# Kernel tuning notes

Hardware: AMD Instinct MI355X
Metric: run time of the kernel (lower is better)

Reference implementation:

```python
import jax, jax.numpy as jnp
import numpy as np

N = 50000
E = 800000
TEXT_VOCAB = 7000
ACTION_DIM = 64
MAX_POS = 5120
POS_DIM = 128   # edge encoder out_dim
NODE_DIM = 128  # text_out 64 + type_out 64
EDGE_DIM = 128
H1 = 256
OUT = 32
NEG_SLOPE = 0.2


def _pos_table():
    # sinusoidal table, [MAX_POS+1, POS_DIM]; even cols = cos, odd cols = sin
    positions = np.arange(0, MAX_POS + 1, dtype=np.float32)
    inv_freq = 1.0 / (10000.0 ** (np.arange(0.0, POS_DIM, 2.0, dtype=np.float32) / POS_DIM))
    si = np.outer(positions, inv_freq)
    tab = np.zeros((MAX_POS + 1, POS_DIM), dtype=np.float32)
    tab[:, 1::2] = np.sin(si)
    tab[:, 0::2] = np.cos(si)
    return jnp.asarray(tab)


def setup_inputs() -> dict:
    key = jax.random.key(0)
    ks = jax.random.split(key, 32)
    ri = jax.random.randint
    nrm = lambda k, s, scale=0.05: (jax.random.normal(k, s, dtype=jnp.float32) * scale)
    x = jnp.stack([ri(ks[0], (N,), 0, TEXT_VOCAB + 1, dtype=jnp.int32),
                   ri(ks[1], (N,), 0, 3, dtype=jnp.int32)], axis=-1)
    edge_index = ri(ks[2], (2, E), 0, N, dtype=jnp.int32)
    edge_attr = jnp.stack([ri(ks[3], (E,), 0, 3, dtype=jnp.int32),
                           ri(ks[4], (E,), 0, MAX_POS + 1, dtype=jnp.int32)], axis=-1)
    d = {
        "x": x, "edge_index": edge_index, "edge_attr": edge_attr,
        "text_emb": nrm(ks[5], (TEXT_VOCAB + 1, 64), 1.0),
        "type_emb": nrm(ks[6], (3, 64), 1.0),
        "flow_emb": nrm(ks[7], (3, EDGE_DIM), 1.0),
        "pos_table": _pos_table(),
        "pos_W": nrm(ks[8], (POS_DIM, POS_DIM)), "pos_b": nrm(ks[9], (POS_DIM,)),
        "c1_Wl": nrm(ks[10], (NODE_DIM, H1)), "c1_bl": nrm(ks[11], (H1,)),
        "c1_Wr": nrm(ks[12], (NODE_DIM, H1)), "c1_br": nrm(ks[13], (H1,)),
        "c1_We": nrm(ks[14], (EDGE_DIM, H1)), "c1_att": nrm(ks[15], (H1,)),
        "c1_bias": nrm(ks[16], (H1,)),
        "c2_Wl": nrm(ks[17], (H1, OUT)), "c2_bl": nrm(ks[18], (OUT,)),
        "c2_Wr": nrm(ks[19], (H1, OUT)), "c2_br": nrm(ks[20], (OUT,)),
        "c2_We": nrm(ks[21], (EDGE_DIM, OUT)), "c2_att": nrm(ks[22], (OUT,)),
        "c2_bias": nrm(ks[23], (OUT,)),
        "policy_W": nrm(ks[24], (OUT, ACTION_DIM), 0.2), "policy_b": nrm(ks[25], (ACTION_DIM,)),
    }
    return d


def gatv2(h, src, dst, ea, Wl, bl, Wr, br, We, att, bias, n):
    # PyG GATv2Conv, heads=1, add_self_loops=True, fill_value='mean'
    loop_attr = jnp.broadcast_to(ea.mean(0), (n, ea.shape[1]))
    s = jnp.concatenate([src, jnp.arange(n, dtype=src.dtype)])
    d = jnp.concatenate([dst, jnp.arange(n, dtype=dst.dtype)])
    ea_full = jnp.concatenate([ea, loop_attr], axis=0)
    xl = h @ Wl + bl  # messages (source side)
    xr = h @ Wr + br  # destination side
    m = xl[s] + xr[d] + ea_full @ We          # [E+n, F]
    e = jnp.where(m > 0, m, NEG_SLOPE * m) @ att  # per-edge logit [E+n]
    emax = jax.ops.segment_max(e, d, num_segments=n)
    a = jnp.exp(e - emax[d])
    denom = jax.ops.segment_sum(a, d, num_segments=n)
    alpha = a / denom[d]
    return jax.ops.segment_sum(alpha[:, None] * xl[s], d, num_segments=n) + bias


def reference(x, edge_index, edge_attr, text_emb, type_emb, flow_emb, pos_table,
              pos_W, pos_b,
              c1_Wl, c1_bl, c1_Wr, c1_br, c1_We, c1_att, c1_bias,
              c2_Wl, c2_bl, c2_Wr, c2_br, c2_We, c2_att, c2_bias,
              policy_W, policy_b):
    # NodeEncoder: concat of text and type embeddings -> [N, 128]
    h = jnp.concatenate([text_emb[x[:, 0]], type_emb[x[:, 1]]], axis=-1)
    # EdgeEncoder: flow embedding + linear(position sinusoid embedding)
    pos = edge_attr[:, 1]
    pos = jnp.where(pos > MAX_POS, pos, MAX_POS)  # faithful to original .where usage
    pos = jnp.clip(pos, 0, MAX_POS)
    ea = flow_emb[edge_attr[:, 0]] + (pos_table[pos] @ pos_W + pos_b)  # [E, 128]
    src, dst = edge_index[0], edge_index[1]
    h = gatv2(h, src, dst, ea, c1_Wl, c1_bl, c1_Wr, c1_br, c1_We, c1_att, c1_bias, h.shape[0])
    h = gatv2(h, src, dst, ea, c2_Wl, c2_bl, c2_Wr, c2_br, c2_We, c2_att, c2_bias, h.shape[0])
    g = h.mean(0)  # [32] graph readout
    logits = g @ policy_W + policy_b
    return jax.nn.softmax(logits, axis=-1)
```

## Files before the change

### kernel.cpp

```cpp
#include <hip/hip_runtime.h>

#define NEG_SLOPE 0.2f

typedef __attribute__((ext_vector_type(8))) short bf16x8;
typedef __attribute__((ext_vector_type(4))) float f32x4;

static __device__ __forceinline__ float wsum64(float v) {
#pragma unroll
    for (int off = 32; off >= 1; off >>= 1) v += __shfl_xor(v, off, 64);
    return v;
}
static __device__ __forceinline__ float wmax64(float v) {
#pragma unroll
    for (int off = 32; off >= 1; off >>= 1) v = fmaxf(v, __shfl_xor(v, off, 64));
    return v;
}

static __device__ __forceinline__ unsigned short bf16r(float a) {
    unsigned int u = __float_as_uint(a);
    return (unsigned short)((u + 0x7FFFu + ((u >> 16) & 1u)) >> 16);
}
static __device__ __forceinline__ unsigned int bf16pack(float a, float b) {
    unsigned int ua = __float_as_uint(a);
    ua = (ua + 0x7FFFu + ((ua >> 16) & 1u)) >> 16;
    unsigned int ub = __float_as_uint(b);
    ub = (ub + 0x7FFFu + ((ub >> 16) & 1u)) & 0xFFFF0000u;
    return ua | ub;
}
static __device__ __forceinline__ float4 bf16x4_to_f4(uint2 u) {
    float4 v;
    v.x = __uint_as_float(u.x << 16);
    v.y = __uint_as_float(u.x & 0xFFFF0000u);
    v.z = __uint_as_float(u.y << 16);
    v.w = __uint_as_float(u.y & 0xFFFF0000u);
    return v;
}

static __device__ __forceinline__ float sdot4(const float4 xs, const float4 pre,
                                              const float4 av6, const float4 av4) {
    float m0 = xs.x + pre.x, m1 = xs.y + pre.y;
    float m2 = xs.z + pre.z, m3 = xs.w + pre.w;
    float q = av6.x * m0 + av4.x * fabsf(m0);
    q = fmaf(av6.y, m1, q); q = fmaf(av4.y, fabsf(m1), q);
    q = fmaf(av6.z, m2, q); q = fmaf(av4.z, fabsf(m2), q);
    q = fmaf(av6.w, m3, q); q = fmaf(av4.w, fabsf(m3), q);
    return q;
}

__global__ void k_edges(const int* __restrict__ ei, const int* __restrict__ ea,
                        int* __restrict__ cntF, int* __restrict__ cnt3, int E) {
    __shared__ int sh3[3];
    if (threadIdx.x < 3) sh3[threadIdx.x] = 0;
    __syncthreads();
    int e = blockIdx.x * blockDim.x + threadIdx.x;
    if (e < E) {
        int dd = ei[E + e];
        int f = ea[2 * e];
        f = f < 0 ? 0 : (f > 2 ? 2 : f);
        atomicAdd(&cntF[dd * 3 + f], 1);
        atomicAdd(&sh3[f], 1);
    }
    __syncthreads();
    if (threadIdx.x < 3) atomicAdd(&cnt3[threadIdx.x], sh3[threadIdx.x]);
}

__global__ void k_prep_all(const float* __restrict__ pos_table, const float* __restrict__ pos_W,
                           const float* __restrict__ pos_b, const float* __restrict__ flow_emb,
                           const float* __restrict__ We1, const float* __restrict__ We2,
                           const int* __restrict__ cnt3,
                           float* __restrict__ eaW1, float* __restrict__ loopW1,
                           float* __restrict__ eaW2, float* __restrict__ loopW2,
                           const float* __restrict__ Wl1, const float* __restrict__ Wr1,
                           const float* __restrict__ Wl2, const float* __restrict__ Wr2,
                           unsigned short* __restrict__ Bt1, unsigned short* __restrict__ Bt2,
                           int E) {
    if (blockIdx.x != 0) {
        int i = (blockIdx.x - 1) * 256 + threadIdx.x;
        if (i < 512 * 128) {
            int nn = i >> 7, k = i & 127;
            float v = (nn < 256) ? Wl1[(size_t)k * 256 + nn] : Wr1[(size_t)k * 256 + nn - 256];
            Bt1[i] = bf16r(v);
        } else {
            int j = i - 512 * 128;
            if (j < 64 * 256) {
                int nn = j >> 8, k = j & 255;
                float v = (nn < 32) ? Wl2[(size_t)k * 32 + nn] : Wr2[(size_t)k * 32 + nn - 32];
                Bt2[j] = bf16r(v);
            }
        }
        return;
    }
    __shared__ float posc[128];
    __shared__ float lv[128];
    int t = threadIdx.x;
    if (t < 128) {
        const float* row = pos_table + 5120 * 128;
        float a = pos_b[t];
        for (int k = 0; k < 128; ++k) a += row[k] * pos_W[k * 128 + t];
        posc[t] = a;
        float invE = 1.0f / (float)E;
        lv[t] = ((float)cnt3[0] * flow_emb[t] + (float)cnt3[1] * flow_emb[128 + t] +
                 (float)cnt3[2] * flow_emb[256 + t]) * invE + a;
    }
    __syncthreads();
    {
        int j = t;
        float a0 = 0.f, a1 = 0.f, a2 = 0.f, al = 0.f;
        for (int k = 0; k < 128; ++k) {
            float w = We1[k * 256 + j];
            float pc = posc[k];
            a0 += (flow_emb[k] + pc) * w;
            a1 += (flow_emb[128 + k] + pc) * w;
            a2 += (flow_emb[256 + k] + pc) * w;
            al += lv[k] * w;
        }
        eaW1[j] = a0; eaW1[256 + j] = a1; eaW1[512 + j] = a2; loopW1[j] = al;
    }
    if (t < 32) {
        int j = t;
        float a0 = 0.f, a1 = 0.f, a2 = 0.f, al = 0.f;
        for (int k = 0; k < 128; ++k) {
            float w = We2[k * 32 + j];
            float pc = posc[k];
            a0 += (flow_emb[k] + pc) * w;
            a1 += (flow_emb[128 + k] + pc) * w;
            a2 += (flow_emb[256 + k] + pc) * w;
            al += lv[k] * w;
        }
        eaW2[j] = a0; eaW2[32 + j] = a1; eaW2[64 + j] = a2; loopW2[j] = al;
    }
}

__global__ __launch_bounds__(256) void k_scan_block(const int* __restrict__ cnt,
                                                    int* __restrict__ rowptr,
                                                    int* __restrict__ bsum, int n) {
    __shared__ int sh[256];
    int b = blockIdx.x, t = threadIdx.x;
    int base = b * 1024 + t * 4;
    int v0 = base + 0 < n ? cnt[base + 0] : 0;
    int v1 = base + 1 < n ? cnt[base + 1] : 0;
    int v2 = base + 2 < n ? cnt[base + 2] : 0;
    int v3 = base + 3 < n ? cnt[base + 3] : 0;
    int tot = v0 + v1 + v2 + v3;
    sh[t] = tot;
    __syncthreads();
    for (int off = 1; off < 256; off <<= 1) {
        int x = (t >= off) ? sh[t - off] : 0;
        __syncthreads();
        sh[t] += x;
        __syncthreads();
    }
    int excl = (t > 0) ? sh[t - 1] : 0;
    if (base + 0 < n) rowptr[base + 0] = excl;
    if (base + 1 < n) rowptr[base + 1] = excl + v0;
    if (base + 2 < n) rowptr[base + 2] = excl + v0 + v1;
    if (base + 3 < n) rowptr[base + 3] = excl + v0 + v1 + v2;
    if (t == 255) bsum[b] = sh[255];
}

__global__ void k_scan_top(int* __restrict__ bsum, int* __restrict__ rowptr, int nb, int n) {
    if (threadIdx.x == 0 && blockIdx.x == 0) {
        int run = 0;
        for (int b = 0; b < nb; ++b) { int x = bsum[b]; bsum[b] = run; run += x; }
        rowptr[n] = run;
    }
}

__global__ void k_scan_add(int* __restrict__ rowptr, const int* __restrict__ bsum,
                           int* __restrict__ wptr, int n) {
    int i = blockIdx.x * blockDim.x + threadIdx.x;
    if (i < n) {
        int v = rowptr[i] + bsum[i >> 10];
        rowptr[i] = v;
        wptr[i] = v;
    }
}

__global__ void k_scatter(const int* __restrict__ ei, const int* __restrict__ ea,
                          int* __restrict__ wptr, int* __restrict__ packed, int E) {
    int e = blockIdx.x * blockDim.x + threadIdx.x;
    if (e >= E) return;
    int s = ei[e], dd = ei[E + e];
    int f = ea[2 * e];
    f = f < 0 ? 0 : (f > 2 ? 2 : f);
    int p = atomicAdd(&wptr[dd * 3 + f], 1);
    packed[p] = s | (f << 16);
}

__global__ __launch_bounds__(256) void k_gemm1(const int* __restrict__ x,
        const float* __restrict__ text_emb, const float* __restrict__ type_emb,
        const unsigned short* __restrict__ Bt,
        const float* __restrict__ bl, const float* __restrict__ br,
        unsigned short* __restrict__ xc, int n) {
    __shared__ unsigned short Ash[64][136];
    __shared__ unsigned short Bsh[128][136];
    int t = threadIdx.x;
    int node0 = blockIdx.x * 64;
    for (int i = t; i < 64 * 128; i += 256) {
        int r = i >> 7, cc = i & 127;
        int nd = node0 + r;
        float v = 0.f;
        if (nd < n)
            v = (cc < 64) ? text_emb[(size_t)x[nd * 2] * 64 + cc]
                          : type_emb[(size_t)x[nd * 2 + 1] * 64 + (cc - 64)];
        Ash[r][cc] = bf16r(v);
    }
    int wave = t >> 6, lane = t & 63;
    int m = lane & 15, q = lane >> 4;
    for (int nb = 0; nb < 4; ++nb) {
        __syncthreads();
        for (int i = t; i < 128 * 16; i += 256) {
            int r = i >> 4, cs = i & 15;
            uint4 v = ((const uint4*)(Bt + (size_t)(nb * 128 + r) * 128))[cs];
            *(uint4*)&Bsh[r][cs * 8] = v;
        }
        __syncthreads();
        f32x4 acc[8];
#pragma unroll
        for (int nt = 0; nt < 8; ++nt) acc[nt] = (f32x4){0.f, 0.f, 0.f, 0.f};
#pragma unroll
        for (int k = 0; k < 128; k += 32) {
            bf16x8 a = *(const bf16x8*)&Ash[wave * 16 + m][k + q * 8];
#pragma unroll
            for (int nt = 0; nt < 8; ++nt) {
                bf16x8 b = *(const bf16x8*)&Bsh[nt * 16 + m][k + q * 8];
                acc[nt] = __builtin_amdgcn_mfma_f32_16x16x32_bf16(a, b, acc[nt], 0, 0, 0);
            }
        }
#pragma unroll
        for (int r = 0; r < 4; ++r) {
            int node = node0 + wave * 16 + q * 4 + r;
            if (node < n) {
                unsigned short* rowp = xc + (size_t)node * 512 + nb * 128 + m;
#pragma unroll
                for (int nt = 0; nt < 8; ++nt) {
                    int ng = nb * 128 + nt * 16 + m;
                    float bv = (ng < 256) ? bl[ng] : br[ng - 256];
                    rowp[nt * 16] = bf16r(acc[nt][r] + bv);
                }
            }
        }
    }
}

__global__ __launch_bounds__(256) void k_gemm2(const unsigned short* __restrict__ h2b,
        const unsigned short* __restrict__ Bt,
        const float* __restrict__ bl, const float* __restrict__ br,
        unsigned short* __restrict__ xc, int n) {
    __shared__ unsigned short Ash[32][264];
    __shared__ unsigned short Bsh[64][264];
    int t = threadIdx.x;
    int node0 = blockIdx.x * 32;
    for (int i = t; i < 32 * 32; i += 256) {
        int r = i >> 5, cs = i & 31;
        int nd = node0 + r;
        uint4 v = make_uint4(0u, 0u, 0u, 0u);
        if (nd < n) v = ((const uint4*)(h2b + (size_t)nd * 256))[cs];
        *(uint4*)&Ash[r][cs * 8] = v;
    }
    for (int i = t; i < 64 * 32; i += 256) {
        int r = i >> 5, cs = i & 31;
        uint4 v = ((const uint4*)(Bt + (size_t)r * 256))[cs];
        *(uint4*)&Bsh[r][cs * 8] = v;
    }
    __syncthreads();
    int wave = t >> 6, lane = t & 63;
    int m = lane & 15, q = lane >> 4;
    int mrow = (wave >> 1) * 16;
    int nh   = (wave & 1) * 32;
    f32x4 acc[2];
    acc[0] = (f32x4){0.f, 0.f, 0.f, 0.f};
    acc[1] = (f32x4){0.f, 0.f, 0.f, 0.f};
#pragma unroll
    for (int k = 0; k < 256; k += 32) {
        bf16x8 a = *(const bf16x8*)&Ash[mrow + m][k + q * 8];
#pragma unroll
        for (int nt = 0; nt < 2; ++nt) {
            bf16x8 b = *(const bf16x8*)&Bsh[nh + nt * 16 + m][k + q * 8];
            acc[nt] = __builtin_amdgcn_mfma_f32_16x16x32_bf16(a, b, acc[nt], 0, 0, 0);
        }
    }
#pragma unroll
    for (int r = 0; r < 4; ++r) {
        int node = node0 + mrow + q * 4 + r;
        if (node < n) {
#pragma unroll
            for (int nt = 0; nt < 2; ++nt) {
                int ng = nh + nt * 16 + m;
                float bv = (ng < 32) ? bl[ng] : br[ng - 32];
                xc[(size_t)node * 64 + ng] = bf16r(acc[nt][r] + bv);
            }
        }
    }
}

__global__ __launch_bounds__(256) void k_gat256(const unsigned short* __restrict__ xc1,
        const int* __restrict__ rowptrF, const int* __restrict__ packed,
        const float* __restrict__ eaW, const float* __restrict__ loopW,
        const float* __restrict__ att, const float* __restrict__ bias,
        unsigned short* __restrict__ h2b, int n) {
    int wid = (blockIdx.x * blockDim.x + threadIdx.x) >> 6;
    int lane = threadIdx.x & 63;
    if (wid >= n) return;
    int d = wid;
    int c = lane * 4;
    float4 xld = bf16x4_to_f4(((const uint2*)(xc1 + (size_t)d * 512))[lane]);
    float4 xrd = bf16x4_to_f4(((const uint2*)(xc1 + (size_t)d * 512 + 256))[lane]);
    float4 av = *(const float4*)(att + c);
    float4 av6, av4;
    av6.x = 0.6f * av.x; av6.y = 0.6f * av.y; av6.z = 0.6f * av.z; av6.w = 0.6f * av.w;
    av4.x = 0.4f * av.x; av4.y = 0.4f * av.y; av4.z = 0.4f * av.z; av4.w = 0.4f * av.w;
    float4 r0 = *(const float4*)(eaW + c);
    float4 r1 = *(const float4*)(eaW + 256 + c);
    float4 r2 = *(const float4*)(eaW + 512 + c);
    r0.x += xrd.x; r0.y += xrd.y; r0.z += xrd.z; r0.w += xrd.w;
    r1.x += xrd.x; r1.y += xrd.y; r1.z += xrd.z; r1.w += xrd.w;
    r2.x += xrd.x; r2.y += xrd.y; r2.z += xrd.z; r2.w += xrd.w;
    float den;
    float4 acc;
    {
        float4 lw = *(const float4*)(loopW + c);
        lw.x += xrd.x; lw.y += xrd.y; lw.z += xrd.z; lw.w += xrd.w;
        float q = wsum64(sdot4(xld, lw, av6, av4));
        float wself = __expf(q);
        den = wself;
        acc.x = wself * xld.x; acc.y = wself * xld.y;
        acc.z = wself * xld.z; acc.w = wself * xld.w;
    }
    int p = rowptrF[d * 3], p1 = rowptrF[d * 3 + 3];
    for (; p + 4 <= p1; p += 4) {
        int pk0 = packed[p],     pk1 = packed[p + 1];
        int pk2 = packed[p + 2], pk3 = packed[p + 3];
        uint2 u0 = ((const uint2*)(xc1 + (size_t)(pk0 & 0xFFFF) * 512))[lane];
        uint2 u1 = ((const uint2*)(xc1 + (size_t)(pk1 & 0xFFFF) * 512))[lane];
        uint2 u2 = ((const uint2*)(xc1 + (size_t)(pk2 & 0xFFFF) * 512))[lane];
        uint2 u3 = ((const uint2*)(xc1 + (size_t)(pk3 & 0xFFFF) * 512))[lane];
        float4 xs0 = bf16x4_to_f4(u0);
        float4 xs1 = bf16x4_to_f4(u1);
        float4 xs2 = bf16x4_to_f4(u2);
        float4 xs3 = bf16x4_to_f4(u3);
        int f0 = pk0 >> 16, f1 = pk1 >> 16, f2 = pk2 >> 16, f3 = pk3 >> 16;
        float4 pr0 = (f0 == 0) ? r0 : ((f0 == 1) ? r1 : r2);
        float4 pr1 = (f1 == 0) ? r0 : ((f1 == 1) ? r1 : r2);
        float4 pr2 = (f2 == 0) ? r0 : ((f2 == 1) ? r1 : r2);
        float4 pr3 = (f3 == 0) ? r0 : ((f3 == 1) ? r1 : r2);
        float q0 = sdot4(xs0, pr0, av6, av4);
        float q1 = sdot4(xs1, pr1, av6, av4);
        float q2 = sdot4(xs2, pr2, av6, av4);
        float q3 = sdot4(xs3, pr3, av6, av4);
#pragma unroll
        for (int off = 32; off >= 1; off >>= 1) {
            q0 += __shfl_xor(q0, off, 64);
            q1 += __shfl_xor(q1, off, 64);
            q2 += __shfl_xor(q2, off, 64);
            q3 += __shfl_xor(q3, off, 64);
        }
        float w0 = __expf(q0), w1 = __expf(q1);
        float w2 = __expf(q2), w3 = __expf(q3);
        den += (w0 + w1) + (w2 + w3);
        acc.x += w0 * xs0.x + w1 * xs1.x + w2 * xs2.x + w3 * xs3.x;
        acc.y += w0 * xs0.y + w1 * xs1.y + w2 * xs2.y + w3 * xs3.y;
        acc.z += w0 * xs0.z + w1 * xs1.z + w2 * xs2.z + w3 * xs3.z;
        acc.w += w0 * xs0.w + w1 * xs1.w + w2 * xs2.w + w3 * xs3.w;
    }
    for (; p < p1; ++p) {
        int pk = packed[p];
        float4 xs = bf16x4_to_f4(((const uint2*)(xc1 + (size_t)(pk & 0xFFFF) * 512))[lane]);
        int f = pk >> 16;
        float4 pr = (f == 0) ? r0 : ((f == 1) ? r1 : r2);
        float qq = wsum64(sdot4(xs, pr, av6, av4));
        float w = __expf(qq);
        den += w;
        acc.x += w * xs.x; acc.y += w * xs.y; acc.z += w * xs.z; acc.w += w * xs.w;
    }
    float inv = 1.f / den;
    float4 bv = *(const float4*)(bias + c);
    float ox = fmaf(acc.x, inv, bv.x), oy = fmaf(acc.y, inv, bv.y);
    float oz = fmaf(acc.z, inv, bv.z), ow = fmaf(acc.w, inv, bv.w);
    ((uint2*)(h2b + (size_t)d * 256))[lane] = make_uint2(bf16pack(ox, oy), bf16pack(oz, ow));
}

__global__ __launch_bounds__(256) void k_gat32(const unsigned short* __restrict__ xc2,
        const int* __restrict__ rowptrF, const int* __restrict__ packed,
        const float* __restrict__ eaW, const float* __restrict__ loopW,
        const float* __restrict__ att, const float* __restrict__ bias,
        float* __restrict__ out, int n) {
    int wid = (blockIdx.x * blockDim.x + threadIdx.x) >> 6;
    if (wid >= n) return;
    int lane = threadIdx.x & 63;
    int g = lane >> 4, li = lane & 15;
    int d = wid;
    unsigned int uxl = ((const unsigned int*)(xc2 + (size_t)d * 64))[li];
    unsigned int uxr = ((const unsigned int*)(xc2 + (size_t)d * 64 + 32))[li];
    float xl0 = __uint_as_float(uxl << 16), xl1 = __uint_as_float(uxl & 0xFFFF0000u);
    float xr0 = __uint_as_float(uxr << 16), xr1 = __uint_as_float(uxr & 0xFFFF0000u);
    float2 avv = ((const float2*)att)[li];
    float a60 = 0.6f * avv.x, a61 = 0.6f * avv.y;
    float a40 = 0.4f * avv.x, a41 = 0.4f * avv.y;
    float2 e0 = ((const float2*)eaW)[li];
    float2 e1 = ((const float2*)(eaW + 32))[li];
    float2 e2 = ((const float2*)(eaW + 64))[li];
    float p00 = e0.x + xr0, p01 = e0.y + xr1;
    float p10 = e1.x + xr0, p11 = e1.y + xr1;
    float p20 = e2.x + xr0, p21 = e2.y + xr1;
    float den, acc0, acc1;
    {
        float2 lwv = ((const float2*)loopW)[li];
        float m0 = xl0 + xr0 + lwv.x, m1 = xl1 + xr1 + lwv.y;
        float q = a60 * m0 + a40 * fabsf(m0);
        q = fmaf(a61, m1, q); q = fmaf(a41, fabsf(m1), q);
        q += __shfl_xor(q, 1, 64); q += __shfl_xor(q, 2, 64);
        q += __shfl_xor(q, 4, 64); q += __shfl_xor(q, 8, 64);
        float wself = __expf(q);
        den  = (g == 0) ? wself : 0.f;
        acc0 = (g == 0) ? wself * xl0 : 0.f;
        acc1 = (g == 0) ? wself * xl1 : 0.f;
    }
    int pA = rowptrF[d * 3], pB = rowptrF[d * 3 + 3];
    int p = pA + g;
    for (; p + 4 < pB; p += 8) {
        int pk0 = packed[p], pk1 = packed[p + 4];
        unsigned int ua = ((const unsigned int*)(xc2 + (size_t)(pk0 & 0xFFFF) * 64))[li];
        unsigned int ub = ((const unsigned int*)(xc2 + (size_t)(pk1 & 0xFFFF) * 64))[li];
        int fA = pk0 >> 16, fB = pk1 >> 16;
        float preA0 = (fA == 0) ? p00 : ((fA == 1) ? p10 : p20);
        float preA1 = (fA == 0) ? p01 : ((fA == 1) ? p11 : p21);
        float preB0 = (fB == 0) ? p00 : ((fB == 1) ? p10 : p20);
        float preB1 = (fB == 0) ? p01 : ((fB == 1) ? p11 : p21);
        float xa0 = __uint_as_float(ua << 16), xa1 = __uint_as_float(ua & 0xFFFF0000u);
        float xb0 = __uint_as_float(ub << 16), xb1 = __uint_as_float(ub & 0xFFFF0000u);
        float ma0 = xa0 + preA0, ma1 = xa1 + preA1;
        float mb0 = xb0 + preB0, mb1 = xb1 + preB1;
        float qa = a60 * ma0 + a40 * fabsf(ma0);
        qa = fmaf(a61, ma1, qa); qa = fmaf(a41, fabsf(ma1), qa);
        float qb = a60 * mb0 + a40 * fabsf(mb0);
        qb = fmaf(a61, mb1, qb); qb = fmaf(a41, fabsf(mb1), qb);
#pragma unroll
        for (int off = 1; off <= 8; off <<= 1) {
            qa += __shfl_xor(qa, off, 64);
            qb += __shfl_xor(qb, off, 64);
        }
        float wa = __expf(qa), wb = __expf(qb);
        den += wa + wb;
        acc0 = fmaf(wb, xb0, fmaf(wa, xa0, acc0));
        acc1 = fmaf(wb, xb1, fmaf(wa, xa1, acc1));
    }
    for (; p < pB; p += 4) {
        int pk = packed[p];
        unsigned int u = ((const unsigned int*)(xc2 + (size_t)(pk & 0xFFFF) * 64))[li];
        int f = pk >> 16;
        float pre0 = (f == 0) ? p00 : ((f == 1) ? p10 : p20);
        float pre1 = (f == 0) ? p01 : ((f == 1) ? p11 : p21);
        float x0 = __uint_as_float(u << 16), x1 = __uint_as_float(u & 0xFFFF0000u);
        float m0 = x0 + pre0, m1 = x1 + pre1;
        float q = a60 * m0 + a40 * fabsf(m0);
        q = fmaf(a61, m1, q); q = fmaf(a41, fabsf(m1), q);
        q += __shfl_xor(q, 1, 64); q += __shfl_xor(q, 2, 64);
        q += __shfl_xor(q, 4, 64); q += __shfl_xor(q, 8, 64);
        float w = __expf(q);
        den += w;
        acc0 = fmaf(w, x0, acc0);
        acc1 = fmaf(w, x1, acc1);
    }
    acc0 += __shfl_xor(acc0, 16, 64); acc0 += __shfl_xor(acc0, 32, 64);
    acc1 += __shfl_xor(acc1, 16, 64); acc1 += __shfl_xor(acc1, 32, 64);
    den  += __shfl_xor(den, 16, 64);  den  += __shfl_xor(den, 32, 64);
    if (g == 0) {
        float2 bvv = ((const float2*)bias)[li];
        float inv = 1.f / den;
        float2 o;
        o.x = fmaf(acc0, inv, bvv.x);
        o.y = fmaf(acc1, inv, bvv.y);
        ((float2*)(out + (size_t)d * 32))[li] = o;
    }
}

__global__ __launch_bounds__(256) void k_mean(const float* __restrict__ out2,
                                              float* __restrict__ gsum, int n) {
    __shared__ float sh[256];
    int t = threadIdx.x;
    int c = t & 31, g = t >> 5;
    float acc = 0.f;
    for (int nd = blockIdx.x * 8 + g; nd < n; nd += gridDim.x * 8)
        acc += out2[(size_t)nd * 32 + c];
    sh[t] = acc;
    __syncthreads();
    if (t < 32) {
        float s2 = 0.f;
#pragma unroll
        for (int gg = 0; gg < 8; ++gg) s2 += sh[gg * 32 + c];
        atomicAdd(&gsum[c], s2);
    }
}

__global__ void k_final(const float* __restrict__ gsum, const float* __restrict__ policy_W,
                        const float* __restrict__ policy_b, float* __restrict__ out, int n) {
    int t = threadIdx.x;
    float invN = 1.0f / (float)n;
    float acc = policy_b[t];
    for (int cc = 0; cc < 32; ++cc) acc += gsum[cc] * invN * policy_W[cc * 64 + t];
    float mx = wmax64(acc);
    float ex = __expf(acc - mx);
    float s = wsum64(ex);
    out[t] = ex / s;
}

extern "C" void kernel_launch(void* const* d_in, const int* in_sizes, int n_in,
                              void* d_out, int out_size, void* d_ws, size_t ws_size,
                              hipStream_t stream) {
    const int* x          = (const int*)d_in[0];
    const int* edge_index = (const int*)d_in[1];
    const int* edge_attr  = (const int*)d_in[2];
    const float* text_emb = (const float*)d_in[3];
    const float* type_emb = (const float*)d_in[4];
    const float* flow_emb = (const float*)d_in[5];
    const float* pos_table= (const float*)d_in[6];
    const float* pos_W    = (const float*)d_in[7];
    const float* pos_b    = (const float*)d_in[8];
    const float* c1_Wl    = (const float*)d_in[9];
    const float* c1_bl    = (const float*)d_in[10];
    const float* c1_Wr    = (const float*)d_in[11];
    const float* c1_br    = (const float*)d_in[12];
    const float* c1_We    = (const float*)d_in[13];
    const float* c1_att   = (const float*)d_in[14];
    const float* c1_bias  = (const float*)d_in[15];
    const float* c2_Wl    = (const float*)d_in[16];
    const float* c2_bl    = (const float*)d_in[17];
    const float* c2_Wr    = (const float*)d_in[18];
    const float* c2_br    = (const float*)d_in[19];
    const float* c2_We    = (const float*)d_in[20];
    const float* c2_att   = (const float*)d_in[21];
    const float* c2_bias  = (const float*)d_in[22];
    const float* policy_W = (const float*)d_in[23];
    const float* policy_b = (const float*)d_in[24];
    float* out = (float*)d_out;

    const int N = in_sizes[0] / 2;
    const int E = in_sizes[1] / 2;
    const int n3 = 3 * N;

    char* base = (char*)d_ws;
    size_t off = 0;
    auto alloc = [&](size_t bytes) -> void* {
        void* p = base + off;
        off = (off + bytes + 255) & ~(size_t)255;
        return p;
    };
    unsigned short* xc1  = (unsigned short*)alloc((size_t)N * 512 * 2);
    unsigned short* h2b  = (unsigned short*)alloc((size_t)N * 256 * 2);
    unsigned short* xc2  = (unsigned short*)alloc((size_t)N * 64 * 2);
    float*          out2 = (float*)alloc((size_t)N * 32 * 4);
    unsigned short* Bt1  = (unsigned short*)alloc((size_t)512 * 128 * 2);
    unsigned short* Bt2  = (unsigned short*)alloc((size_t)64 * 256 * 2);
    int*            zreg   = (int*)alloc((size_t)(n3 + 36) * 4);
    int*            cntF   = zreg;
    int*            cnt3   = zreg + n3;
    float*          gsum   = (float*)(zreg + n3 + 4);
    int*            rowptrF= (int*)alloc((size_t)(n3 + 1) * 4);
    int*            packed = (int*)alloc((size_t)E * 4);
    int*            bsum   = (int*)alloc(256 * 4);
    float*          eaW1   = (float*)alloc(768 * 4);
    float*          loopW1 = (float*)alloc(256 * 4);
    float*          eaW2   = (float*)alloc(96 * 4);
    float*          loopW2 = (float*)alloc(32 * 4);

    hipMemsetAsync(zreg, 0, (size_t)(n3 + 36) * 4, stream);

    k_edges<<<(E + 255) / 256, 256, 0, stream>>>(edge_index, edge_attr, cntF, cnt3, E);
    k_prep_all<<<1 + (512 * 128 + 64 * 256) / 256, 256, 0, stream>>>(
        pos_table, pos_W, pos_b, flow_emb, c1_We, c2_We, cnt3,
        eaW1, loopW1, eaW2, loopW2, c1_Wl, c1_Wr, c2_Wl, c2_Wr, Bt1, Bt2, E);

    int nb = (n3 + 1023) / 1024;
    k_scan_block<<<nb, 256, 0, stream>>>(cntF, rowptrF, bsum, n3);
    k_scan_top<<<1, 64, 0, stream>>>(bsum, rowptrF, nb, n3);
    k_scan_add<<<(n3 + 255) / 256, 256, 0, stream>>>(rowptrF, bsum, cntF, n3);
    k_scatter<<<(E + 255) / 256, 256, 0, stream>>>(edge_index, edge_attr, cntF, packed, E);

    k_gemm1<<<(N + 63) / 64, 256, 0, stream>>>(x, text_emb, type_emb, Bt1,
                                               c1_bl, c1_br, xc1, N);
    k_gat256<<<(N + 3) / 4, 256, 0, stream>>>(xc1, rowptrF, packed, eaW1, loopW1,
                                              c1_att, c1_bias, h2b, N);

    k_gemm2<<<(N + 31) / 32, 256, 0, stream>>>(h2b, Bt2, c2_bl, c2_br, xc2, N);
    k_gat32<<<(N + 3) / 4, 256, 0, stream>>>(xc2, rowptrF, packed, eaW2, loopW2,
                                             c2_att, c2_bias, out2, N);

    k_mean<<<256, 256, 0, stream>>>(out2, gsum, N);
    k_final<<<1, 64, 0, stream>>>(gsum, policy_W, policy_b, out, N);
}
```

Before: 431.6 us.

## Split leaky-relu attention score into precomputed linear part and abs part

Uses leaky_relu(m)=0.6m+0.4|m| to move the linear term of the layer-1 attention score into per-node (alpha) and per-flow-type (delta) scalars, computed by a new k_alpha256 kernel. The per-edge inner loop then only evaluates the abs term plus a scalar gather, and the log2e scaling is folded in so exp2f can replace __expf. It also adds readfirstlane on the node index and a uniform-flow fast path. The cost is an extra kernel launch, an N-float buffer, and one extra scalar gather per edge.

```diff
diff --git a/kernel.cpp b/kernel.cpp
--- a/kernel.cpp
+++ b/kernel.cpp
@@ -1,9 +1,9 @@
 #include <hip/hip_runtime.h>
-
-#define NEG_SLOPE 0.2f
 
 typedef __attribute__((ext_vector_type(8))) short bf16x8;
 typedef __attribute__((ext_vector_type(4))) float f32x4;
+
+#define L2E 1.4426950408889634f
 
 static __device__ __forceinline__ float wsum64(float v) {
 #pragma unroll
@@ -35,15 +35,18 @@
     v.w = __uint_as_float(u.y & 0xFFFF0000u);
     return v;
 }
-
-static __device__ __forceinline__ float sdot4(const float4 xs, const float4 pre,
-                                              const float4 av6, const float4 av4) {
+static __device__ __forceinline__ float rflf(float v) {
+    return __int_as_float(__builtin_amdgcn_readfirstlane(__float_as_int(v)));
+}
+
+static __device__ __forceinline__ float adot4(const float4 xs, const float4 pre,
+                                              const float4 av4) {
     float m0 = xs.x + pre.x, m1 = xs.y + pre.y;
     float m2 = xs.z + pre.z, m3 = xs.w + pre.w;
-    float q = av6.x * m0 + av4.x * fabsf(m0);
-    q = fmaf(av6.y, m1, q); q = fmaf(av4.y, fabsf(m1), q);
-    q = fmaf(av6.z, m2, q); q = fmaf(av4.z, fabsf(m2), q);
-    q = fmaf(av6.w, m3, q); q = fmaf(av4.w, fabsf(m3), q);
+    float q = av4.x * fabsf(m0);
+    q = fmaf(av4.y, fabsf(m1), q);
+    q = fmaf(av4.z, fabsf(m2), q);
+    q = fmaf(av4.w, fabsf(m3), q);
     return q;
 }
 
@@ -294,35 +297,69 @@
     }
 }
 
+__global__ __launch_bounds__(256) void k_alpha256(const unsigned short* __restrict__ xc1,
+        const float* __restrict__ att, const float* __restrict__ eaW,
+        const float* __restrict__ loopW, float* __restrict__ alpha,
+        float* __restrict__ delta, int n) {
+    const float S6 = 0.6f * L2E;
+    int lane = threadIdx.x & 63;
+    int c = lane * 4;
+    float4 av = *(const float4*)(att + c);
+    int wid = (blockIdx.x * blockDim.x + threadIdx.x) >> 6;
+    if (wid < n) {
+        float4 xl = bf16x4_to_f4(((const uint2*)(xc1 + (size_t)wid * 512))[lane]);
+        float q = av.x * xl.x;
+        q = fmaf(av.y, xl.y, q); q = fmaf(av.z, xl.z, q); q = fmaf(av.w, xl.w, q);
+        q = wsum64(q);
+        if (lane == 0) alpha[wid] = q * S6;
+    } else if (wid < n + 4) {
+        int f = wid - n;
+        const float* src = (f < 3) ? (eaW + f * 256) : loopW;
+        float4 v = *(const float4*)(src + c);
+        float q = av.x * v.x;
+        q = fmaf(av.y, v.y, q); q = fmaf(av.z, v.z, q); q = fmaf(av.w, v.w, q);
+        q = wsum64(q);
+        if (lane == 0) delta[f] = q * S6;
+    }
+}
+
 __global__ __launch_bounds__(256) void k_gat256(const unsigned short* __restrict__ xc1,
         const int* __restrict__ rowptrF, const int* __restrict__ packed,
         const float* __restrict__ eaW, const float* __restrict__ loopW,
         const float* __restrict__ att, const float* __restrict__ bias,
+        const float* __restrict__ alpha, const float* __restrict__ delta,
         unsigned short* __restrict__ h2b, int n) {
     int wid = (blockIdx.x * blockDim.x + threadIdx.x) >> 6;
+    if (wid >= n) return;
+    int d = __builtin_amdgcn_readfirstlane(wid);
     int lane = threadIdx.x & 63;
-    if (wid >= n) return;
-    int d = wid;
     int c = lane * 4;
+    const float S4 = 0.4f * L2E;
+    const float S6 = 0.6f * L2E;
     float4 xld = bf16x4_to_f4(((const uint2*)(xc1 + (size_t)d * 512))[lane]);
     float4 xrd = bf16x4_to_f4(((const uint2*)(xc1 + (size_t)d * 512 + 256))[lane]);
     float4 av = *(const float4*)(att + c);
-    float4 av6, av4;
-    av6.x = 0.6f * av.x; av6.y = 0.6f * av.y; av6.z = 0.6f * av.z; av6.w = 0.6f * av.w;
-    av4.x = 0.4f * av.x; av4.y = 0.4f * av.y; av4.z = 0.4f * av.z; av4.w = 0.4f * av.w;
+    float4 av4;
+    av4.x = S4 * av.x; av4.y = S4 * av.y; av4.z = S4 * av.z; av4.w = S4 * av.w;
+    float gq = av.x * xrd.x;
+    gq = fmaf(av.y, xrd.y, gq); gq = fmaf(av.z, xrd.z, gq); gq = fmaf(av.w, xrd.w, gq);
+    float gd = rflf(wsum64(gq) * S6);
+    float ab0 = gd + delta[0], ab1 = gd + delta[1], ab2 = gd + delta[2];
+    float ab3 = gd + delta[3];
+    float alphad = alpha[d];
     float4 r0 = *(const float4*)(eaW + c);
     float4 r1 = *(const float4*)(eaW + 256 + c);
     float4 r2 = *(const float4*)(eaW + 512 + c);
+    float4 lwp = *(const float4*)(loopW + c);
     r0.x += xrd.x; r0.y += xrd.y; r0.z += xrd.z; r0.w += xrd.w;
     r1.x += xrd.x; r1.y += xrd.y; r1.z += xrd.z; r1.w += xrd.w;
     r2.x += xrd.x; r2.y += xrd.y; r2.z += xrd.z; r2.w += xrd.w;
+    lwp.x += xrd.x; lwp.y += xrd.y; lwp.z += xrd.z; lwp.w += xrd.w;
     float den;
     float4 acc;
     {
-        float4 lw = *(const float4*)(loopW + c);
-        lw.x += xrd.x; lw.y += xrd.y; lw.z += xrd.z; lw.w += xrd.w;
-        float q = wsum64(sdot4(xld, lw, av6, av4));
-        float wself = __expf(q);
+        float q = wsum64(adot4(xld, lwp, av4)) + alphad + ab3;
+        float wself = exp2f(q);
         den = wself;
         acc.x = wself * xld.x; acc.y = wself * xld.y;
         acc.z = wself * xld.z; acc.w = wself * xld.w;
@@ -331,23 +368,38 @@
     for (; p + 4 <= p1; p += 4) {
         int pk0 = packed[p],     pk1 = packed[p + 1];
         int pk2 = packed[p + 2], pk3 = packed[p + 3];
-        uint2 u0 = ((const uint2*)(xc1 + (size_t)(pk0 & 0xFFFF) * 512))[lane];
-        uint2 u1 = ((const uint2*)(xc1 + (size_t)(pk1 & 0xFFFF) * 512))[lane];
-        uint2 u2 = ((const uint2*)(xc1 + (size_t)(pk2 & 0xFFFF) * 512))[lane];
-        uint2 u3 = ((const uint2*)(xc1 + (size_t)(pk3 & 0xFFFF) * 512))[lane];
+        int s0 = pk0 & 0xFFFF, s1 = pk1 & 0xFFFF;
+        int s2 = pk2 & 0xFFFF, s3 = pk3 & 0xFFFF;
+        int f0 = pk0 >> 16, f1 = pk1 >> 16, f2 = pk2 >> 16, f3 = pk3 >> 16;
+        uint2 u0 = ((const uint2*)(xc1 + (size_t)s0 * 512))[lane];
+        uint2 u1 = ((const uint2*)(xc1 + (size_t)s1 * 512))[lane];
+        uint2 u2 = ((const uint2*)(xc1 + (size_t)s2 * 512))[lane];
+        uint2 u3 = ((const uint2*)(xc1 + (size_t)s3 * 512))[lane];
+        float sc0 = alpha[s0] + ((f0 == 0) ? ab0 : ((f0 == 1) ? ab1 : ab2));
+        float sc1 = alpha[s1] + ((f1 == 0) ? ab0 : ((f1 == 1) ? ab1 : ab2));
+        float sc2 = alpha[s2] + ((f2 == 0) ? ab0 : ((f2 == 1) ? ab1 : ab2));
+        float sc3 = alpha[s3] + ((f3 == 0) ? ab0 : ((f3 == 1) ? ab1 : ab2));
         float4 xs0 = bf16x4_to_f4(u0);
         float4 xs1 = bf16x4_to_f4(u1);
         float4 xs2 = bf16x4_to_f4(u2);
         float4 xs3 = bf16x4_to_f4(u3);
-        int f0 = pk0 >> 16, f1 = pk1 >> 16, f2 = pk2 >> 16, f3 = pk3 >> 16;
-        float4 pr0 = (f0 == 0) ? r0 : ((f0 == 1) ? r1 : r2);
-        float4 pr1 = (f1 == 0) ? r0 : ((f1 == 1) ? r1 : r2);
-        float4 pr2 = (f2 == 0) ? r0 : ((f2 == 1) ? r1 : r2);
-        float4 pr3 = (f3 == 0) ? r0 : ((f3 == 1) ? r1 : r2);
-        float q0 = sdot4(xs0, pr0, av6, av4);
-        float q1 = sdot4(xs1, pr1, av6, av4);
-        float q2 = sdot4(xs2, pr2, av6, av4);
-        float q3 = sdot4(xs3, pr3, av6, av4);
+        float q0, q1, q2, q3;
+        if (f0 == f3) {
+            float4 pr = (f0 == 0) ? r0 : ((f0 == 1) ? r1 : r2);
+            q0 = adot4(xs0, pr, av4);
+            q1 = adot4(xs1, pr, av4);
+            q2 = adot4(xs2, pr, av4);
+            q3 = adot4(xs3, pr, av4);
+        } else {
+            float4 pr0 = (f0 == 0) ? r0 : ((f0 == 1) ? r1 : r2);
+            float4 pr1 = (f1 == 0) ? r0 : ((f1 == 1) ? r1 : r2);
+            float4 pr2 = (f2 == 0) ? r0 : ((f2 == 1) ? r1 : r2);
+            float4 pr3 = (f3 == 0) ? r0 : ((f3 == 1) ? r1 : r2);
+            q0 = adot4(xs0, pr0, av4);
+            q1 = adot4(xs1, pr1, av4);
+            q2 = adot4(xs2, pr2, av4);
+            q3 = adot4(xs3, pr3, av4);
+        }
 #pragma unroll
         for (int off = 32; off >= 1; off >>= 1) {
             q0 += __shfl_xor(q0, off, 64);
@@ -355,8 +407,8 @@
             q2 += __shfl_xor(q2, off, 64);
             q3 += __shfl_xor(q3, off, 64);
         }
-        float w0 = __expf(q0), w1 = __expf(q1);
-        float w2 = __expf(q2), w3 = __expf(q3);
+        float w0 = exp2f(q0 + sc0), w1 = exp2f(q1 + sc1);
+        float w2 = exp2f(q2 + sc2), w3 = exp2f(q3 + sc3);
         den += (w0 + w1) + (w2 + w3);
         acc.x += w0 * xs0.x + w1 * xs1.x + w2 * xs2.x + w3 * xs3.x;
         acc.y += w0 * xs0.y + w1 * xs1.y + w2 * xs2.y + w3 * xs3.y;
@@ -365,11 +417,13 @@
     }
     for (; p < p1; ++p) {
         int pk = packed[p];
-        float4 xs = bf16x4_to_f4(((const uint2*)(xc1 + (size_t)(pk & 0xFFFF) * 512))[lane]);
-        int f = pk >> 16;
+        int s = pk & 0xFFFF, f = pk >> 16;
+        uint2 u = ((const uint2*)(xc1 + (size_t)s * 512))[lane];
+        float sc = alpha[s] + ((f == 0) ? ab0 : ((f == 1) ? ab1 : ab2));
+        float4 xs = bf16x4_to_f4(u);
         float4 pr = (f == 0) ? r0 : ((f == 1) ? r1 : r2);
-        float qq = wsum64(sdot4(xs, pr, av6, av4));
-        float w = __expf(qq);
+        float q = wsum64(adot4(xs, pr, av4)) + sc;
+        float w = exp2f(q);
         den += w;
         acc.x += w * xs.x; acc.y += w * xs.y; acc.z += w * xs.z; acc.w += w * xs.w;
     }
@@ -387,16 +441,16 @@
         float* __restrict__ out, int n) {
     int wid = (blockIdx.x * blockDim.x + threadIdx.x) >> 6;
     if (wid >= n) return;
+    int d = __builtin_amdgcn_readfirstlane(wid);
     int lane = threadIdx.x & 63;
     int g = lane >> 4, li = lane & 15;
-    int d = wid;
     unsigned int uxl = ((const unsigned int*)(xc2 + (size_t)d * 64))[li];
     unsigned int uxr = ((const unsigned int*)(xc2 + (size_t)d * 64 + 32))[li];
     float xl0 = __uint_as_float(uxl << 16), xl1 = __uint_as_float(uxl & 0xFFFF0000u);
     float xr0 = __uint_as_float(uxr << 16), xr1 = __uint_as_float(uxr & 0xFFFF0000u);
     float2 avv = ((const float2*)att)[li];
-    float a60 = 0.6f * avv.x, a61 = 0.6f * avv.y;
-    float a40 = 0.4f * avv.x, a41 = 0.4f * avv.y;
+    float a60 = 0.6f * L2E * avv.x, a61 = 0.6f * L2E * avv.y;
+    float a40 = 0.4f * L2E * avv.x, a41 = 0.4f * L2E * avv.y;
     float2 e0 = ((const float2*)eaW)[li];
     float2 e1 = ((const float2*)(eaW + 32))[li];
     float2 e2 = ((const float2*)(eaW + 64))[li];
@@ -411,7 +465,7 @@
         q = fmaf(a61, m1, q); q = fmaf(a41, fabsf(m1), q);
         q += __shfl_xor(q, 1, 64); q += __shfl_xor(q, 2, 64);
         q += __shfl_xor(q, 4, 64); q += __shfl_xor(q, 8, 64);
-        float wself = __expf(q);
+        float wself = exp2f(q);
         den  = (g == 0) ? wself : 0.f;
         acc0 = (g == 0) ? wself * xl0 : 0.f;
         acc1 = (g == 0) ? wself * xl1 : 0.f;
@@ -440,7 +494,7 @@
             qa += __shfl_xor(qa, off, 64);
             qb += __shfl_xor(qb, off, 64);
         }
-        float wa = __expf(qa), wb = __expf(qb);
+        float wa = exp2f(qa), wb = exp2f(qb);
         den += wa + wb;
         acc0 = fmaf(wb, xb0, fmaf(wa, xa0, acc0));
         acc1 = fmaf(wb, xb1, fmaf(wa, xa1, acc1));
@@ -457,7 +511,7 @@
         q = fmaf(a61, m1, q); q = fmaf(a41, fabsf(m1), q);
         q += __shfl_xor(q, 1, 64); q += __shfl_xor(q, 2, 64);
         q += __shfl_xor(q, 4, 64); q += __shfl_xor(q, 8, 64);
-        float w = __expf(q);
+        float w = exp2f(q);
         den += w;
         acc0 = fmaf(w, x0, acc0);
         acc1 = fmaf(w, x1, acc1);
@@ -552,6 +606,8 @@
     float*          out2 = (float*)alloc((size_t)N * 32 * 4);
     unsigned short* Bt1  = (unsigned short*)alloc((size_t)512 * 128 * 2);
     unsigned short* Bt2  = (unsigned short*)alloc((size_t)64 * 256 * 2);
+    float*          alpha1 = (float*)alloc((size_t)N * 4);
+    float*          delta1 = (float*)alloc(4 * 4);
     int*            zreg   = (int*)alloc((size_t)(n3 + 36) * 4);
     int*            cntF   = zreg;
     int*            cnt3   = zreg + n3;
@@ -579,8 +635,10 @@
 
     k_gemm1<<<(N + 63) / 64, 256, 0, stream>>>(x, text_emb, type_emb, Bt1,
                                                c1_bl, c1_br, xc1, N);
+    k_alpha256<<<(N + 4 + 3) / 4, 256, 0, stream>>>(xc1, c1_att, eaW1, loopW1,
+                                                    alpha1, delta1, N);
     k_gat256<<<(N + 3) / 4, 256, 0, stream>>>(xc1, rowptrF, packed, eaW1, loopW1,
-                                              c1_att, c1_bias, h2b, N);
+                                              c1_att, c1_bias, alpha1, delta1, h2b, N);
 
     k_gemm2<<<(N + 31) / 32, 256, 0, stream>>>(h2b, Bt2, c2_bl, c2_br, xc2, N);
     k_gat32<<<(N + 3) / 4, 256, 0, stream>>>(xc2, rowptrF, packed, eaW2, loopW2,
```

Result: no change. 432.9 us (+0.3%).
